# Optimization experiments

Hardware: AMD Instinct MI355X
Metric: run time of the kernel (lower is better)

Reference implementation:

```python
import jax, jax.numpy as jnp
import numpy as np

KS = 3
N_TAPS = KS * KS
PAD = 1
EPS = 1e-5


def conv2d(x, w, b=None, stride=1, padding=1):
    out = jax.lax.conv_general_dilated(
        x, w, (stride, stride), [(padding, padding), (padding, padding)],
        dimension_numbers=('NCHW', 'OIHW', 'NCHW'))
    if b is not None:
        out = out + b[None, :, None, None]
    return out


def deform_conv(x, p_conv_w, p_conv_b, dcn_w):
    # x: (b,c,H,W). Canonical pure-torch DCNv1 (no modulation), stride=1, padding=1.
    off = conv2d(x, p_conv_w, p_conv_b, 1, 1).transpose(0, 2, 3, 1)  # (b,h,w,2N)
    b, h, w, _ = off.shape
    xp = jnp.pad(x, ((0, 0), (0, 0), (PAD, PAD), (PAD, PAD)))  # zero-pad
    Hp, Wp = xp.shape[2], xp.shape[3]
    r = jnp.arange(-(KS - 1) // 2, (KS - 1) // 2 + 1, dtype=x.dtype)
    pn_h, pn_w = [a.reshape(-1) for a in jnp.meshgrid(r, r, indexing='ij')]  # (N,)
    p0_h = jnp.arange(1, h + 1, dtype=x.dtype)[:, None, None]  # (h,1,1)
    p0_w = jnp.arange(1, w + 1, dtype=x.dtype)[None, :, None]  # (1,w,1)
    ph = jnp.clip(p0_h + pn_h + off[..., :N_TAPS], 0, Hp - 1)   # (b,h,w,N)
    pw = jnp.clip(p0_w + pn_w + off[..., N_TAPS:], 0, Wp - 1)
    fh, fw = jnp.floor(ph), jnp.floor(pw)
    lt_h = jnp.clip(fh, 0, Hp - 1); lt_w = jnp.clip(fw, 0, Wp - 1)
    rb_h = jnp.clip(fh + 1, 0, Hp - 1); rb_w = jnp.clip(fw + 1, 0, Wp - 1)
    g_lt = (1 + (lt_h - ph)) * (1 + (lt_w - pw))
    g_rb = (1 - (rb_h - ph)) * (1 - (rb_w - pw))
    g_lb = (1 + (lt_h - ph)) * (1 - (rb_w - pw))
    g_rt = (1 - (rb_h - ph)) * (1 + (lt_w - pw))
    ilt_h, ilt_w = lt_h.astype(jnp.int32), lt_w.astype(jnp.int32)
    irb_h, irb_w = rb_h.astype(jnp.int32), rb_w.astype(jnp.int32)
    gather = jax.vmap(lambda im, iy, ix: im[:, iy, ix])  # per-sample -> (c,h,w,N)
    x_lt = gather(xp, ilt_h, ilt_w)
    x_rb = gather(xp, irb_h, irb_w)
    x_lb = gather(xp, ilt_h, irb_w)
    x_rt = gather(xp, irb_h, ilt_w)
    xo = (g_lt[:, None] * x_lt + g_rb[:, None] * x_rb +
          g_lb[:, None] * x_lb + g_rt[:, None] * x_rt)  # (b,c,h,w,N)
    O, C = dcn_w.shape[0], dcn_w.shape[1]
    # reshape-to-(h*ks,w*ks) + stride-ks conv == contraction over tap n = ky*ks+kx
    return jnp.einsum('bchwn,ocn->bohw', xo, dcn_w.reshape(O, C, N_TAPS))


def batchnorm(x, gamma, beta):
    mu = x.mean((0, 2, 3), keepdims=True)
    var = ((x - mu) ** 2).mean((0, 2, 3), keepdims=True)  # biased var (torch BN)
    return gamma[None, :, None, None] * (x - mu) * jax.lax.rsqrt(var + EPS) + beta[None, :, None, None]


def setup_inputs() -> dict:
    key = jax.random.key(0)
    ks = jax.random.split(key, 8)
    B, C, O, H, W = 8, 64, 128, 128, 128
    return {
        'x': jax.random.normal(ks[0], (B, C, H, W), jnp.float32),
        'p_conv_w': jax.random.normal(ks[1], (2 * N_TAPS, C, 3, 3), jnp.float32) * 0.01,
        'p_conv_b': jax.random.normal(ks[2], (2 * N_TAPS,), jnp.float32) * 0.1,
        'dcn_w': jax.random.normal(ks[3], (C, C, 3, 3), jnp.float32) * 0.05,
        'bn_gamma': jnp.ones((C,), jnp.float32) + 0.1 * jax.random.normal(ks[4], (C,), jnp.float32),
        'bn_beta': 0.1 * jax.random.normal(ks[5], (C,), jnp.float32),
        'conv2_w': jax.random.normal(ks[6], (O, C, 3, 3), jnp.float32) * 0.05,
        'conv2_b': jax.random.normal(ks[7], (O,), jnp.float32) * 0.05,
    }


def reference(x, p_conv_w, p_conv_b, dcn_w, bn_gamma, bn_beta, conv2_w, conv2_b):
    out = deform_conv(x, p_conv_w, p_conv_b, dcn_w)
    out = jax.nn.relu(batchnorm(out, bn_gamma, bn_beta))
    out = out + x
    return conv2d(out, conv2_w, conv2_b, 1, 1)  # (B, 128, 128, 128)
```

## Files before the change

### kernel.cpp

```cpp
#include <hip/hip_runtime.h>
#include <hip/hip_bf16.h>

#define BB 8
#define CC 64
#define OO 128
#define HH 128
#define WW 128
#define HW (HH*WW)
#define NTAP 9

typedef float f32x4 __attribute__((ext_vector_type(4)));
typedef short short8 __attribute__((ext_vector_type(8)));

__device__ __forceinline__ uint f2bf(float v) {
    uint b = __float_as_uint(v);
    return (b + 0x7FFFu + ((b >> 16) & 1u)) >> 16;
}

__device__ __forceinline__ float sampf(const float* __restrict__ xc, int iy, int ix) {
    unsigned uy = (unsigned)(iy - 1), ux = (unsigned)(ix - 1);
    return (uy < 128u && ux < 128u) ? xc[uy * 128 + ux] : 0.f;
}

__global__ void k_repack(const float* __restrict__ pw, const float* __restrict__ dw,
                         const float* __restrict__ cw,
                         float* __restrict__ wp1, float* __restrict__ wpd,
                         ushort* __restrict__ wb2) {
    int i = blockIdx.x * 256 + threadIdx.x;
    if (i < 10368) {
        int o = i % 18, t = (i / 18) % 9, c = i / 162;
        wp1[i] = pw[(o * 64 + c) * 9 + t];
    }
    if (i < 36864) {
        int o = i % 64, t = (i / 64) % 9, c = i / 576;
        wpd[i] = dw[(o * 64 + c) * 9 + t];
    }
    if (i < 73728) {
        int j = i & 7, lane = (i >> 3) & 63, ot = (i >> 9) & 7;
        int kc = (i >> 12) & 1, t = i >> 13;
        int c = kc * 32 + (lane >> 4) * 8 + j;
        int oc = ot * 16 + (lane & 15);
        wb2[i] = (ushort)f2bf(cw[(oc * 64 + c) * 9 + t]);
    }
}

__global__ __launch_bounds__(256) void k_pconv(const float* __restrict__ x,
                                               const float* __restrict__ wp1,
                                               const float* __restrict__ pb,
                                               float* __restrict__ off) {
    int tile = blockIdx.x;
    int b = blockIdx.y;
    int ty0 = (tile / 8) * 16, tx0 = (tile % 8) * 16;
    int tid = threadIdx.x;
    int py = tid / 16, px = tid % 16;
    __shared__ float lx[16][18 * 18];

    float acc[18];
#pragma unroll
    for (int o = 0; o < 18; o++) acc[o] = pb[o];

    for (int cc = 0; cc < 4; cc++) {
        __syncthreads();
        for (int idx = tid; idx < 16 * 324; idx += 256) {
            int c = idx / 324, r = (idx % 324) / 18, col = idx % 18;
            int gy = ty0 + r - 1, gx = tx0 + col - 1;
            float v = 0.f;
            if ((unsigned)gy < 128u && (unsigned)gx < 128u)
                v = x[((b * 64 + cc * 16 + c) * 128 + gy) * 128 + gx];
            lx[c][r * 18 + col] = v;
        }
        __syncthreads();
        for (int c = 0; c < 16; c++) {
#pragma unroll
            for (int t = 0; t < 9; t++) {
                float xv = lx[c][(py + t / 3) * 18 + px + t % 3];
                const float* wr = wp1 + ((cc * 16 + c) * 9 + t) * 18;
#pragma unroll
                for (int o = 0; o < 18; o++) acc[o] = fmaf(xv, wr[o], acc[o]);
            }
        }
    }
    int yy = ty0 + py, xx = tx0 + px;
#pragma unroll
    for (int o = 0; o < 18; o++)
        off[((b * 18 + o) * 128 + yy) * 128 + xx] = acc[o];
}

__global__ __launch_bounds__(256) void k_deform(const float* __restrict__ x,
                                                const float* __restrict__ off,
                                                const float* __restrict__ wpd,
                                                float* __restrict__ y) {
    int tile = blockIdx.x;
    int b = blockIdx.y;
    int ty0 = (tile / 16) * 8, tx0 = (tile % 16) * 8;
    int tid = threadIdx.x;

    __shared__ uint   mwin[576];
    __shared__ float4 mwt[576];
    __shared__ float  xtile[4 * 256];
    __shared__ float  xo[4][580];

    for (int e = tid; e < 576; e += 256) {
        int n = e >> 6, p = e & 63;
        int py = p >> 3, px = p & 7;
        int yy = ty0 + py, xx = tx0 + px;
        float offh = off[((b * 18 + n) * 128 + yy) * 128 + xx];
        float offw = off[((b * 18 + 9 + n) * 128 + yy) * 128 + xx];
        float ph = (float)(yy + 1) + (float)(n / 3 - 1) + offh;
        float pw = (float)(xx + 1) + (float)(n % 3 - 1) + offw;
        ph = fminf(fmaxf(ph, 0.f), 129.f);
        pw = fminf(fmaxf(pw, 0.f), 129.f);
        float fh = floorf(ph), fw = floorf(pw);
        int lth = (int)fh, ltw = (int)fw;
        int rbh = min(lth + 1, 129), rbw = min(ltw + 1, 129);
        float dh_l = 1.f + (fh - ph);
        float dh_r = 1.f - ((float)rbh - ph);
        float dw_l = 1.f + (fw - pw);
        float dw_r = 1.f - ((float)rbw - pw);
        int uy0 = lth - 1, ux0 = ltw - 1, uy1 = rbh - 1, ux1 = rbw - 1;
        bool iy0 = (unsigned)uy0 < 128u, ix0 = (unsigned)ux0 < 128u;
        bool iy1 = (unsigned)uy1 < 128u, ix1 = (unsigned)ux1 < 128u;
        float w_lt = (iy0 && ix0) ? dh_l * dw_l : 0.f;
        float w_rb = (iy1 && ix1) ? dh_r * dw_r : 0.f;
        float w_lb = (iy0 && ix1) ? dh_l * dw_r : 0.f;
        float w_rt = (iy1 && ix0) ? dh_r * dw_l : 0.f;
        mwt[e] = make_float4(w_lt, w_rb, w_lb, w_rt);
        int wy0 = uy0 - ty0 + 4, wx0 = ux0 - tx0 + 4;
        int wy1 = uy1 - ty0 + 4, wx1 = ux1 - tx0 + 4;
        uint win = 0xFFFFFFFFu;
        if ((unsigned)wy0 < 16u && (unsigned)wx0 < 16u &&
            (unsigned)wy1 < 16u && (unsigned)wx1 < 16u) {
            uint o00 = (uint)(wy0 * 16 + wx0);
            uint o11 = (uint)(wy1 * 16 + wx1);
            uint o01 = (uint)(wy0 * 16 + wx1);
            uint o10 = (uint)(wy1 * 16 + wx0);
            win = o00 | (o11 << 8) | (o01 << 16) | (o10 << 24);
        }
        mwin[e] = win;
    }

    float acc[16] = {};
    int cg = tid >> 6;
    int l64 = tid & 63;
    int cgoff = cg * 256;
    int ob = __builtin_amdgcn_readfirstlane(cg * 16);

    for (int cc = 0; cc < 16; cc++) {
#pragma unroll
        for (int i2 = 0; i2 < 4; i2++) {
            int idx = tid + 256 * i2;
            int c = idx >> 8, wp = idx & 255;
            int gy = ty0 - 4 + (wp >> 4), gx = tx0 - 4 + (wp & 15);
            float v = 0.f;
            if ((unsigned)gy < 128u && (unsigned)gx < 128u)
                v = x[(size_t)(b * 64 + cc * 4 + c) * HW + gy * 128 + gx];
            xtile[idx] = v;
        }
        __syncthreads();
#pragma unroll 2
        for (int i = 0; i < 9; i++) {
            int e = l64 + 64 * i;
            uint w = mwin[e];
            float4 g = mwt[e];
            float v;
            if (__builtin_expect(w != 0xFFFFFFFFu, 1)) {
                float a00 = xtile[cgoff + (w & 255u)];
                float a11 = xtile[cgoff + ((w >> 8) & 255u)];
                float a01 = xtile[cgoff + ((w >> 16) & 255u)];
                float a10 = xtile[cgoff + (w >> 24)];
                v = g.x * a00 + g.y * a11 + g.z * a01 + g.w * a10;
            } else {
                int n = e >> 6, p = e & 63;
                int yy2 = ty0 + (p >> 3), xx2 = tx0 + (p & 7);
                float offh = off[((b * 18 + n) * 128 + yy2) * 128 + xx2];
                float offw = off[((b * 18 + 9 + n) * 128 + yy2) * 128 + xx2];
                float ph = fminf(fmaxf((float)(yy2 + 1) + (float)(n / 3 - 1) + offh, 0.f), 129.f);
                float pw = fminf(fmaxf((float)(xx2 + 1) + (float)(n % 3 - 1) + offw, 0.f), 129.f);
                int lth = (int)floorf(ph), ltw = (int)floorf(pw);
                int rbh = min(lth + 1, 129), rbw = min(ltw + 1, 129);
                const float* xc = x + (size_t)(b * 64 + cc * 4 + cg) * HW;
                v = g.x * sampf(xc, lth, ltw) + g.y * sampf(xc, rbh, rbw)
                  + g.z * sampf(xc, lth, rbw) + g.w * sampf(xc, rbh, ltw);
            }
            xo[cg][e] = v;
        }
        __syncthreads();
        for (int c = 0; c < 4; c++) {
#pragma unroll
            for (int n = 0; n < 9; n++) {
                float xv = xo[c][n * 64 + l64];
                const float* wrow = wpd + (((cc * 4 + c) * 9 + n) * 64) + ob;
#pragma unroll
                for (int j = 0; j < 16; j++)
                    acc[j] = fmaf(xv, wrow[j], acc[j]);
            }
        }
        __syncthreads();
    }

    int yy = ty0 + (l64 >> 3), xx = tx0 + (l64 & 7);
#pragma unroll
    for (int j = 0; j < 16; j++)
        y[(size_t)(b * 64 + ob + j) * HW + yy * 128 + xx] = acc[j];
}

__global__ __launch_bounds__(256) void k_bnpart(const float* __restrict__ y,
                                                float* __restrict__ part) {
    int c = blockIdx.x, b = blockIdx.y;
    int tid = threadIdx.x;
    const float4* p = (const float4*)(y + (size_t)(b * 64 + c) * HW);
    float s = 0.f, sq = 0.f;
    for (int i = tid; i < HW / 4; i += 256) {
        float4 v = p[i];
        s += v.x + v.y + v.z + v.w;
        sq += v.x * v.x + v.y * v.y + v.z * v.z + v.w * v.w;
    }
#pragma unroll
    for (int o = 32; o > 0; o >>= 1) {
        s += __shfl_down(s, o);
        sq += __shfl_down(sq, o);
    }
    __shared__ float rs[4], rq[4];
    int wid = tid >> 6;
    if ((tid & 63) == 0) { rs[wid] = s; rq[wid] = sq; }
    __syncthreads();
    if (tid == 0) {
        part[(b * 64 + c) * 2]     = rs[0] + rs[1] + rs[2] + rs[3];
        part[(b * 64 + c) * 2 + 1] = rq[0] + rq[1] + rq[2] + rq[3];
    }
}

__global__ void k_bnfinal(const float* __restrict__ part,
                          const float* __restrict__ gamma,
                          const float* __restrict__ beta,
                          float* __restrict__ ss) {
    int c = threadIdx.x;
    float s = 0.f, sq = 0.f;
#pragma unroll
    for (int b = 0; b < 8; b++) {
        s += part[(b * 64 + c) * 2];
        sq += part[(b * 64 + c) * 2 + 1];
    }
    const float inv = 1.f / (float)(8 * HW);
    float mean = s * inv;
    float var = sq * inv - mean * mean;
    float scale = gamma[c] * rsqrtf(var + 1e-5f);
    ss[c] = scale;
    ss[64 + c] = beta[c] - mean * scale;
}

__global__ __launch_bounds__(256) void k_conv2(const float* __restrict__ x,
                                               const float* __restrict__ y,
                                               const float* __restrict__ ss,
                                               const ushort* __restrict__ wb2,
                                               const float* __restrict__ b2,
                                               float* __restrict__ out) {
    int tile = blockIdx.x, b = blockIdx.y;
    int ty0 = (tile / 16) * 8, tx0 = (tile % 16) * 8;
    int tid = threadIdx.x;

    __shared__ uint lz[3600];

    for (int idx = tid; idx < 3200; idx += 256) {
        int q = idx / 100, pos = idx % 100;
        int r = pos / 10, col = pos % 10;
        int gy = ty0 + r - 1, gx = tx0 + col - 1;
        uint u = 0;
        if ((unsigned)gy < 128u && (unsigned)gx < 128u) {
            int c0 = q * 2;
            int gi = ((b * 64 + c0) * HW) + gy * 128 + gx;
            float t0 = fmaf(y[gi], ss[c0], ss[64 + c0]);
            float v0 = fmaxf(t0, 0.f) + x[gi];
            float t1 = fmaf(y[gi + HW], ss[c0 + 1], ss[65 + c0]);
            float v1 = fmaxf(t1, 0.f) + x[gi + HW];
            u = (f2bf(v1) << 16) | f2bf(v0);
        }
        lz[pos * 36 + q] = u;
    }
    __syncthreads();

    int lane = tid & 63, pg = tid >> 6;
    int r16 = lane & 15, jg = lane >> 4;
    int p = pg * 16 + r16;
    int pyA = p >> 3, pxA = p & 7;

    f32x4 acc[8];
#pragma unroll
    for (int ot = 0; ot < 8; ot++) {
        float bv = b2[ot * 16 + r16];
        acc[ot] = (f32x4){bv, bv, bv, bv};
    }

#pragma unroll
    for (int t = 0; t < 9; t++) {
        int pos = (pyA + t / 3) * 10 + (pxA + t % 3);
#pragma unroll
        for (int kc = 0; kc < 2; kc++) {
            short8 av = *(const short8*)(lz + pos * 36 + kc * 16 + jg * 4);
            const ushort* wk = wb2 + (t * 2 + kc) * 4096 + lane * 8;
#pragma unroll
            for (int ot = 0; ot < 8; ot++) {
                short8 bv = *(const short8*)(wk + ot * 512);
                acc[ot] = __builtin_amdgcn_mfma_f32_16x16x32_bf16(av, bv, acc[ot], 0, 0, 0);
            }
        }
    }

    int p0 = pg * 16 + jg * 4;
    int yy = ty0 + (p0 >> 3), xx = tx0 + (p0 & 7);
#pragma unroll
    for (int ot = 0; ot < 8; ot++) {
        int oc = ot * 16 + r16;
        *(f32x4*)(out + (size_t)(b * 128 + oc) * HW + yy * 128 + xx) = acc[ot];
    }
}

extern "C" void kernel_launch(void* const* d_in, const int* in_sizes, int n_in,
                              void* d_out, int out_size, void* d_ws, size_t ws_size,
                              hipStream_t stream) {
    const float* x     = (const float*)d_in[0];
    const float* pw    = (const float*)d_in[1];
    const float* pb    = (const float*)d_in[2];
    const float* dw    = (const float*)d_in[3];
    const float* gamma = (const float*)d_in[4];
    const float* beta  = (const float*)d_in[5];
    const float* cw    = (const float*)d_in[6];
    const float* cb    = (const float*)d_in[7];
    float* out = (float*)d_out;
    float* ws  = (float*)d_ws;

    float*  wp1  = ws;
    float*  ss   = ws + 10368;
    float*  part = ws + 10496;
    float*  wpd  = ws + 11520;
    ushort* wb2  = (ushort*)(ws + 48384);
    float*  off  = ws + 85248;
    float*  yb   = ws + 2444544;

    k_repack<<<dim3(288), dim3(256), 0, stream>>>(pw, dw, cw, wp1, wpd, wb2);
    k_pconv<<<dim3(64, 8), dim3(256), 0, stream>>>(x, wp1, pb, off);
    k_deform<<<dim3(256, 8), dim3(256), 0, stream>>>(x, off, wpd, yb);
    k_bnpart<<<dim3(64, 8), dim3(256), 0, stream>>>(yb, part);
    k_bnfinal<<<dim3(1), dim3(64), 0, stream>>>(part, gamma, beta, ss);
    k_conv2<<<dim3(256, 8), dim3(256), 0, stream>>>(x, yb, ss, wb2, cb, out);
}
```

Baseline: 369.6 us.

## Pack two channels as bf16 pairs in shared tiles, halving channel-loop iterations

The deformable conv kernel now stores the input tile and the sampled values in shared memory as packed bf16 pairs, two channels per 32-bit word. The channel loop runs 8 times with 8 channels per pass instead of 16 times with 4. This halves barrier and loop overhead and lets one LDS read serve two channels. The cost is bf16 rounding of the inputs and sampled values, which adds numeric error, plus extra unpack and convert ALU work.

```diff
diff --git a/kernel.cpp b/kernel.cpp
--- a/kernel.cpp
+++ b/kernel.cpp
@@ -97,8 +97,8 @@
 
     __shared__ uint   mwin[576];
     __shared__ float4 mwt[576];
-    __shared__ float  xtile[4 * 256];
-    __shared__ float  xo[4][580];
+    __shared__ uint   xtile[4 * 256];
+    __shared__ uint   xo[4][580];
 
     for (int e = tid; e < 576; e += 256) {
         int n = e >> 6, p = e & 63;
@@ -145,16 +145,20 @@
     int cgoff = cg * 256;
     int ob = __builtin_amdgcn_readfirstlane(cg * 16);
 
-    for (int cc = 0; cc < 16; cc++) {
-#pragma unroll
-        for (int i2 = 0; i2 < 4; i2++) {
-            int idx = tid + 256 * i2;
-            int c = idx >> 8, wp = idx & 255;
-            int gy = ty0 - 4 + (wp >> 4), gx = tx0 - 4 + (wp & 15);
-            float v = 0.f;
-            if ((unsigned)gy < 128u && (unsigned)gx < 128u)
-                v = x[(size_t)(b * 64 + cc * 4 + c) * HW + gy * 128 + gx];
-            xtile[idx] = v;
+    int sgy = ty0 - 4 + (tid >> 4), sgx = tx0 - 4 + (tid & 15);
+    bool sinb = ((unsigned)sgy < 128u && (unsigned)sgx < 128u);
+    int spos = sgy * 128 + sgx;
+
+    for (int cc = 0; cc < 8; cc++) {
+#pragma unroll
+        for (int q = 0; q < 4; q++) {
+            int c0 = cc * 8 + 2 * q;
+            float v0 = 0.f, v1 = 0.f;
+            if (sinb) {
+                v0 = x[(size_t)(b * 64 + c0) * HW + spos];
+                v1 = x[(size_t)(b * 64 + c0 + 1) * HW + spos];
+            }
+            xtile[q * 256 + tid] = (f2bf(v1) << 16) | f2bf(v0);
         }
         __syncthreads();
 #pragma unroll 2
@@ -162,13 +166,18 @@
             int e = l64 + 64 * i;
             uint w = mwin[e];
             float4 g = mwt[e];
-            float v;
+            float vlo, vhi;
             if (__builtin_expect(w != 0xFFFFFFFFu, 1)) {
-                float a00 = xtile[cgoff + (w & 255u)];
-                float a11 = xtile[cgoff + ((w >> 8) & 255u)];
-                float a01 = xtile[cgoff + ((w >> 16) & 255u)];
-                float a10 = xtile[cgoff + (w >> 24)];
-                v = g.x * a00 + g.y * a11 + g.z * a01 + g.w * a10;
+                uint u00 = xtile[cgoff + (w & 255u)];
+                uint u11 = xtile[cgoff + ((w >> 8) & 255u)];
+                uint u01 = xtile[cgoff + ((w >> 16) & 255u)];
+                uint u10 = xtile[cgoff + (w >> 24)];
+                float a00l = __uint_as_float(u00 << 16), a00h = __uint_as_float(u00 & 0xFFFF0000u);
+                float a11l = __uint_as_float(u11 << 16), a11h = __uint_as_float(u11 & 0xFFFF0000u);
+                float a01l = __uint_as_float(u01 << 16), a01h = __uint_as_float(u01 & 0xFFFF0000u);
+                float a10l = __uint_as_float(u10 << 16), a10h = __uint_as_float(u10 & 0xFFFF0000u);
+                vlo = g.x * a00l + g.y * a11l + g.z * a01l + g.w * a10l;
+                vhi = g.x * a00h + g.y * a11h + g.z * a01h + g.w * a10h;
             } else {
                 int n = e >> 6, p = e & 63;
                 int yy2 = ty0 + (p >> 3), xx2 = tx0 + (p & 7);
@@ -178,21 +187,28 @@
                 float pw = fminf(fmaxf((float)(xx2 + 1) + (float)(n % 3 - 1) + offw, 0.f), 129.f);
                 int lth = (int)floorf(ph), ltw = (int)floorf(pw);
                 int rbh = min(lth + 1, 129), rbw = min(ltw + 1, 129);
-                const float* xc = x + (size_t)(b * 64 + cc * 4 + cg) * HW;
-                v = g.x * sampf(xc, lth, ltw) + g.y * sampf(xc, rbh, rbw)
-                  + g.z * sampf(xc, lth, rbw) + g.w * sampf(xc, rbh, ltw);
-            }
-            xo[cg][e] = v;
-        }
-        __syncthreads();
-        for (int c = 0; c < 4; c++) {
+                const float* xc0 = x + (size_t)(b * 64 + cc * 8 + 2 * cg) * HW;
+                const float* xc1 = xc0 + HW;
+                vlo = g.x * sampf(xc0, lth, ltw) + g.y * sampf(xc0, rbh, rbw)
+                    + g.z * sampf(xc0, lth, rbw) + g.w * sampf(xc0, rbh, ltw);
+                vhi = g.x * sampf(xc1, lth, ltw) + g.y * sampf(xc1, rbh, rbw)
+                    + g.z * sampf(xc1, lth, rbw) + g.w * sampf(xc1, rbh, ltw);
+            }
+            xo[cg][e] = (f2bf(vhi) << 16) | f2bf(vlo);
+        }
+        __syncthreads();
+        for (int q = 0; q < 4; q++) {
 #pragma unroll
             for (int n = 0; n < 9; n++) {
-                float xv = xo[c][n * 64 + l64];
-                const float* wrow = wpd + (((cc * 4 + c) * 9 + n) * 64) + ob;
-#pragma unroll
-                for (int j = 0; j < 16; j++)
-                    acc[j] = fmaf(xv, wrow[j], acc[j]);
+                uint u = xo[q][n * 64 + l64];
+                float xlo = __uint_as_float(u << 16);
+                float xhi = __uint_as_float(u & 0xFFFF0000u);
+                const float* w0 = wpd + (((cc * 8 + 2 * q) * 9 + n) * 64) + ob;
+                const float* w1 = w0 + 576;
+#pragma unroll
+                for (int j = 0; j < 16; j++) acc[j] = fmaf(xlo, w0[j], acc[j]);
+#pragma unroll
+                for (int j = 0; j < 16; j++) acc[j] = fmaf(xhi, w1[j], acc[j]);
             }
         }
         __syncthreads();
```

Result: faster. 350.5 us (-5.2%).
